# Kernel tuning notes

Measured on AMD Instinct MI355X. Metric: run time of the kernel, lower is better.

The kernel has to match this reference:

```python
import jax, jax.numpy as jnp
import numpy as np

N, H, W, C = 4, 64, 64, 256
G, K = 8, 3
GC = C // G
P = K * K
PAD = 1
BN_EPS = 1e-3  # ultralytics Conv uses BatchNorm2d(eps=0.001)


def setup_inputs() -> dict:
    key = jax.random.key(0)
    ks = jax.random.split(key, 8)
    return {
        "x": jax.random.normal(ks[0], (N, H, W, C), jnp.float32),
        # depthwise conv weight (OIHW with I=1, feature_group_count=C)
        "dw_w": jax.random.normal(ks[1], (C, 1, K, K), jnp.float32) * 0.1,
        "bn_gamma": jnp.ones((C,), jnp.float32),
        "bn_beta": jnp.zeros((C,), jnp.float32),
        "bn_mean": jnp.zeros((C,), jnp.float32),
        "bn_var": jnp.ones((C,), jnp.float32),
        # offset/mask heads are zero-init in torch; use small random weights so
        # sampling locations are nontrivial but stay near the kernel grid
        "W_off": jax.random.normal(ks[2], (C, G * P * 2), jnp.float32) * 0.01,
        "b_off": jnp.zeros((G * P * 2,), jnp.float32),
        "W_mask": jax.random.normal(ks[3], (C, G * P), jnp.float32) * 0.01,
        "b_mask": jnp.zeros((G * P,), jnp.float32),
        "W_in": jax.random.normal(ks[4], (C, C), jnp.float32) / np.sqrt(C).astype(np.float32),
        "b_in": jnp.zeros((C,), jnp.float32),
        "W_out": jax.random.normal(ks[5], (C, C), jnp.float32) / np.sqrt(C).astype(np.float32),
        "b_out": jnp.zeros((C,), jnp.float32),
    }


def _grid_sample(img, grid):
    # img: (B, gc, Hi, Wi); grid: (B, L, P, 2) in [-1,1], (x,y) order.
    # Matches torch grid_sample(mode='bilinear', padding_mode='zeros', align_corners=False).
    B, gc, Hi, Wi = img.shape
    x = (grid[..., 0] + 1.0) * (Wi * 0.5) - 0.5
    y = (grid[..., 1] + 1.0) * (Hi * 0.5) - 0.5
    x0 = jnp.floor(x).astype(jnp.int32)
    y0 = jnp.floor(y).astype(jnp.int32)
    tx = x - x0
    ty = y - y0
    flat = img.reshape(B, gc, Hi * Wi)
    L, Pp = grid.shape[1], grid.shape[2]

    def tap(xi, yi, w):
        valid = (xi >= 0) & (xi < Wi) & (yi >= 0) & (yi < Hi)
        idx = jnp.clip(yi, 0, Hi - 1) * Wi + jnp.clip(xi, 0, Wi - 1)
        v = jnp.take_along_axis(flat, idx.reshape(B, 1, L * Pp), axis=2)
        v = v.reshape(B, gc, L, Pp)
        return v * (w * valid)[:, None]

    return (tap(x0, y0, (1 - tx) * (1 - ty))
            + tap(x0 + 1, y0, tx * (1 - ty))
            + tap(x0, y0 + 1, (1 - tx) * ty)
            + tap(x0 + 1, y0 + 1, tx * ty))


def _dcnv3_core(xp, offset, mask):
    # xp: (N,H,W,C) projected input; offset: (N,H,W,G*P*2); mask: (N,H,W,G*P)
    xpad = jnp.pad(xp, ((0, 0), (PAD, PAD), (PAD, PAD), (0, 0)))
    Hi, Wi = H + 2 * PAD, W + 2 * PAD
    # reference points on the padded grid, normalized to [0,1]
    start = (K - 1) // 2 + 0.5  # dilation=1, stride=1
    ref_y = (start + jnp.arange(H, dtype=jnp.float32)) / Hi
    ref_x = (start + jnp.arange(W, dtype=jnp.float32)) / Wi
    ref = jnp.stack(jnp.broadcast_arrays(ref_x[None, :], ref_y[:, None]), -1)  # (H,W,2) (x,y)
    # kernel dilation grid; torch meshgrid('ij') over (kw,kh) -> point p = iw*K + ih
    xv = jnp.arange(K, dtype=jnp.float32) - ((K - 1) // 2)
    gx, gy = jnp.meshgrid(xv / Wi, xv / Hi, indexing='ij')
    kgrid = jnp.stack([gx, gy], -1).reshape(P, 2)  # identical per group
    off = offset.reshape(N, H, W, G, P, 2) / jnp.array([Wi, Hi], jnp.float32)
    loc = ref[None, :, :, None, None, :] + kgrid[None, None, None, None] + off  # (N,H,W,G,P,2)
    sg = 2.0 * loc - 1.0
    # regroup channels-last input to (N*G, GC, Hi, Wi); channel c = g*GC + d
    img = xpad.reshape(N, Hi * Wi, G, GC).transpose(0, 2, 3, 1).reshape(N * G, GC, Hi, Wi)
    sgrid = sg.reshape(N, H * W, G, P, 2).transpose(0, 2, 1, 3, 4).reshape(N * G, H * W, P, 2)
    samp = _grid_sample(img, sgrid)  # (N*G, GC, L, P)
    m = mask.reshape(N, H * W, G, P).transpose(0, 2, 1, 3).reshape(N * G, 1, H * W, P)
    out = (samp * m).sum(-1)  # (N*G, GC, L)
    return out.reshape(N, C, H * W).transpose(0, 2, 1).reshape(N, H, W, C)


def reference(x, dw_w, bn_gamma, bn_beta, bn_mean, bn_var, W_off, b_off,
              W_mask, b_mask, W_in, b_in, W_out, b_out):
    x_proj = x @ W_in + b_in
    # depthwise 3x3 conv + BN (eval) + SiLU (ultralytics Conv)
    xc = x.transpose(0, 3, 1, 2)
    y = jax.lax.conv_general_dilated(
        xc, dw_w, (1, 1), ((PAD, PAD), (PAD, PAD)),
        feature_group_count=C, dimension_numbers=('NCHW', 'OIHW', 'NCHW'))
    scale = bn_gamma / jnp.sqrt(bn_var + BN_EPS)
    y = (y - bn_mean[None, :, None, None]) * scale[None, :, None, None] + bn_beta[None, :, None, None]
    y = y * jax.nn.sigmoid(y)
    x1 = y.transpose(0, 2, 3, 1)  # (N,H,W,C)
    offset = x1 @ W_off + b_off
    mlog = (x1 @ W_mask + b_mask).reshape(N, H, W, G, P)
    mask = jax.nn.softmax(mlog, axis=-1).reshape(N, H, W, G * P)
    out = _dcnv3_core(x_proj, offset, mask)
    return out @ W_out + b_out
```

## Files before the change

kernel.cpp:

```cpp
#include <hip/hip_runtime.h>
#include <math.h>

#define NPIX 16384
#define CC 256
#define OFFW 144
#define MSKW 72

typedef unsigned short ushortT;
typedef __attribute__((ext_vector_type(4))) float f32x4;
typedef __attribute__((ext_vector_type(8))) short short8;
typedef __attribute__((ext_vector_type(8))) __bf16 bf16x8;

__device__ __forceinline__ float bf2f(ushortT u) {
    union { unsigned u; float f; } x; x.u = ((unsigned)u) << 16; return x.f;
}
__device__ __forceinline__ ushortT f2bf(float f) {
    union { float f; unsigned u; } x; x.f = f;
    unsigned u = x.u;
    return (ushortT)((u + 0x7FFFu + ((u >> 16) & 1u)) >> 16);
}

typedef __attribute__((address_space(3))) char lds_char;
typedef __attribute__((address_space(1))) char glb_char;
__device__ __forceinline__ void gload_lds16(const void* g, void* l) {
    __builtin_amdgcn_global_load_lds((const glb_char*)g, (lds_char*)l, 16, 0, 0);
}

__global__ __launch_bounds__(256) void k_wt(
    const float* __restrict__ W_in, const float* __restrict__ W_out,
    const float* __restrict__ W_off, const float* __restrict__ W_mask,
    const float* __restrict__ b_in, const float* __restrict__ b_out,
    const float* __restrict__ b_off, const float* __restrict__ b_mask,
    ushortT* __restrict__ Wt, float* __restrict__ biasb)
{
    const int idx = blockIdx.x * 256 + threadIdx.x;
    const int slot = idx >> 16;
    const int rem = idx & 65535;
    const int n = rem >> 8, k = rem & 255;
    float v;
    if (slot == 0)      v = W_in[k * 256 + n];
    else if (slot == 1) v = W_out[k * 256 + n];
    else {
        if (n < OFFW)            v = W_off[k * OFFW + n];
        else if (n < OFFW + MSKW) v = W_mask[k * MSKW + (n - OFFW)];
        else                     v = 0.f;
    }
    Wt[idx] = f2bf(v);
    if (n == 0) {
        float b;
        if (slot == 0)      b = b_in[k];
        else if (slot == 1) b = b_out[k];
        else                b = (k < OFFW) ? b_off[k] : (k < OFFW + MSKW ? b_mask[k - OFFW] : 0.f);
        biasb[slot * 256 + k] = b;
    }
}

__global__ __launch_bounds__(256) void k_pre(
    const float* __restrict__ x, const float* __restrict__ dw_w,
    const float* __restrict__ bn_gamma, const float* __restrict__ bn_beta,
    const float* __restrict__ bn_mean, const float* __restrict__ bn_var,
    ushortT* __restrict__ xb, ushortT* __restrict__ x1b)
{
    __shared__ float xs[30][CC];
    const int tid = threadIdx.x;
    const int base = blockIdx.x * 8;
    const int n = base >> 12, h = (base >> 6) & 63, w0 = base & 63;

    #pragma unroll
    for (int v = 0; v < 30; ++v) {
        const int r = h - 1 + v / 10;
        const int col = w0 - 1 + v % 10;
        float val = 0.f;
        if ((unsigned)r < 64u && (unsigned)col < 64u)
            val = x[(((size_t)n * 64 + r) * 64 + col) * CC + tid];
        xs[v][tid] = val;
    }
    __syncthreads();

    float wreg[9];
    #pragma unroll
    for (int kk = 0; kk < 9; ++kk) wreg[kk] = dw_w[tid * 9 + kk];
    const float scale = bn_gamma[tid] * rsqrtf(bn_var[tid] + 1e-3f);
    const float mean = bn_mean[tid], beta = bn_beta[tid];

    #pragma unroll
    for (int t = 0; t < 8; ++t) {
        float acc = 0.f;
        #pragma unroll
        for (int kh = 0; kh < 3; ++kh)
            #pragma unroll
            for (int kw = 0; kw < 3; ++kw)
                acc += xs[kh * 10 + t + kw][tid] * wreg[kh * 3 + kw];
        float yv = (acc - mean) * scale + beta;
        float s = yv / (1.f + __expf(-yv));
        x1b[(size_t)(base + t) * CC + tid] = f2bf(s);
        xb[(size_t)(base + t) * CC + tid] = f2bf(xs[10 + t + 1][tid]);
    }
}

template <int OUT_BF16>
__global__ __launch_bounds__(256) void k_gemm(
    const ushortT* __restrict__ A, const ushortT* __restrict__ Bt,
    const float* __restrict__ bias, void* __restrict__ Cout)
{
    __shared__ ushortT As[64 * 64];
    __shared__ ushortT Bs[64 * 64];
    const int tid = threadIdx.x;
    const int lane = tid & 63, wave = tid >> 6;
    const int mt = blockIdx.x >> 2, nt = blockIdx.x & 3;
    const int m0 = mt * 64, n0 = nt * 64;
    const int wr = wave >> 1, wc = wave & 1;

    f32x4 acc[2][2];
    #pragma unroll
    for (int i = 0; i < 2; ++i)
        #pragma unroll
        for (int j = 0; j < 2; ++j) acc[i][j] = (f32x4){0.f, 0.f, 0.f, 0.f};

    for (int k0 = 0; k0 < 256; k0 += 64) {
        #pragma unroll
        for (int it = 0; it < 2; ++it) {
            const int i = tid + it * 256;
            const int row = i >> 3, ch = i & 7;
            const int sch = ch ^ (row & 7);
            const int ldsoff = it * 4096 + wave * 1024;
            gload_lds16(A + (size_t)(m0 + row) * 256 + k0 + sch * 8, (char*)As + ldsoff);
            gload_lds16(Bt + (size_t)(n0 + row) * 256 + k0 + sch * 8, (char*)Bs + ldsoff);
        }
        __syncthreads();

        #pragma unroll
        for (int kk = 0; kk < 64; kk += 32) {
            bf16x8 af[2], bf[2];
            #pragma unroll
            for (int m = 0; m < 2; ++m) {
                const int rowl = wr * 32 + m * 16 + (lane & 15);
                const int colb = (kk + (lane >> 4) * 8) * 2;
                af[m] = *(const bf16x8*)((const char*)As + rowl * 128 + (colb ^ ((rowl & 7) << 4)));
            }
            #pragma unroll
            for (int nn = 0; nn < 2; ++nn) {
                const int rowl = wc * 32 + nn * 16 + (lane & 15);
                const int colb = (kk + (lane >> 4) * 8) * 2;
                bf[nn] = *(const bf16x8*)((const char*)Bs + rowl * 128 + (colb ^ ((rowl & 7) << 4)));
            }
            #pragma unroll
            for (int m = 0; m < 2; ++m)
                #pragma unroll
                for (int nn = 0; nn < 2; ++nn)
                    acc[m][nn] = __builtin_amdgcn_mfma_f32_16x16x32_bf16(af[m], bf[nn], acc[m][nn], 0, 0, 0);
        }
        __syncthreads();
    }

    const int rbase = (lane >> 4) * 4, col16 = lane & 15;
    #pragma unroll
    for (int m = 0; m < 2; ++m) {
        #pragma unroll
        for (int nn = 0; nn < 2; ++nn) {
            const int col = n0 + wc * 32 + nn * 16 + col16;
            const float bj = bias[col];
            #pragma unroll
            for (int r = 0; r < 4; ++r) {
                const int row = m0 + wr * 32 + m * 16 + rbase + r;
                const float v = acc[m][nn][r] + bj;
                if (OUT_BF16) ((ushortT*)Cout)[(size_t)row * 256 + col] = f2bf(v);
                else          ((float*)Cout)[(size_t)row * 256 + col] = v;
            }
        }
    }
}

__global__ __launch_bounds__(256) void k_core(
    const float* __restrict__ om, const ushortT* __restrict__ xpb,
    ushortT* __restrict__ coreb)
{
    __shared__ float offL[8][CC];
    __shared__ float msk[8][MSKW];
    __shared__ float wtab[576][8];
    const int tid = threadIdx.x;
    const int base = blockIdx.x * 8;
    const int n = base >> 12, h = (base >> 6) & 63, w0 = base & 63;

    for (int i = tid; i < 8 * CC; i += 256)
        offL[i >> 8][i & 255] = om[(size_t)base * CC + i];
    __syncthreads();

    if (tid < 64) {
        const int t = tid >> 3, g = tid & 7;
        float mx = -1e30f;
        #pragma unroll
        for (int p = 0; p < 9; ++p) mx = fmaxf(mx, offL[t][OFFW + g * 9 + p]);
        float e[9], sum = 0.f;
        #pragma unroll
        for (int p = 0; p < 9; ++p) { e[p] = __expf(offL[t][OFFW + g * 9 + p] - mx); sum += e[p]; }
        const float inv = 1.f / sum;
        #pragma unroll
        for (int p = 0; p < 9; ++p) msk[t][g * 9 + p] = e[p] * inv;
    }
    __syncthreads();

    for (int it = tid; it < 576; it += 256) {
        const int t = it / 72, gp = it % 72, p = gp % 9;
        const float ox = offL[t][gp * 2], oy = offL[t][gp * 2 + 1];
        const float m = msk[t][gp];
        const float px = (float)(w0 + t + p / 3) + ox;
        const float py = (float)(h + p % 3) + oy;
        const float xf = floorf(px), yf = floorf(py);
        const float tx = px - xf, ty = py - yf;
        const int x0 = (int)xf - 1, y0 = (int)yf - 1;
        const int x1 = x0 + 1, y1 = y0 + 1;
        const float wx0 = ((unsigned)x0 < 64u) ? (1.f - tx) : 0.f;
        const float wx1 = ((unsigned)x1 < 64u) ? tx : 0.f;
        const float wy0 = ((unsigned)y0 < 64u) ? (1.f - ty) : 0.f;
        const float wy1 = ((unsigned)y1 < 64u) ? ty : 0.f;
        const int cx0 = min(max(x0, 0), 63), cx1 = min(max(x1, 0), 63);
        const int cy0 = min(max(y0, 0), 63), cy1 = min(max(y1, 0), 63);
        wtab[it][0] = __int_as_float((cy0 * 64 + cx0) * 256);
        wtab[it][1] = __int_as_float((cy0 * 64 + cx1) * 256);
        wtab[it][2] = __int_as_float((cy1 * 64 + cx0) * 256);
        wtab[it][3] = __int_as_float((cy1 * 64 + cx1) * 256);
        wtab[it][4] = m * wx0 * wy0;
        wtab[it][5] = m * wx1 * wy0;
        wtab[it][6] = m * wx0 * wy1;
        wtab[it][7] = m * wx1 * wy1;
    }
    __syncthreads();

    const int g = tid >> 5, d = tid & 31;
    const int c = g * 32 + d;
    const ushortT* xn = xpb + (size_t)n * 4096 * 256 + c;
    #pragma unroll
    for (int t = 0; t < 8; ++t) {
        float acc = 0.f;
        #pragma unroll
        for (int p = 0; p < 9; ++p) {
            const float* wt = wtab[t * 72 + g * 9 + p];
            const int4 o4 = *(const int4*)(wt);
            const float4 w4 = *(const float4*)(wt + 4);
            acc += w4.x * bf2f(xn[o4.x]) + w4.y * bf2f(xn[o4.y])
                 + w4.z * bf2f(xn[o4.z]) + w4.w * bf2f(xn[o4.w]);
        }
        coreb[(size_t)(base + t) * CC + c] = f2bf(acc);
    }
}

extern "C" void kernel_launch(void* const* d_in, const int* in_sizes, int n_in,
                              void* d_out, int out_size, void* d_ws, size_t ws_size,
                              hipStream_t stream) {
    const float* x        = (const float*)d_in[0];
    const float* dw_w     = (const float*)d_in[1];
    const float* bn_gamma = (const float*)d_in[2];
    const float* bn_beta  = (const float*)d_in[3];
    const float* bn_mean  = (const float*)d_in[4];
    const float* bn_var   = (const float*)d_in[5];
    const float* W_off    = (const float*)d_in[6];
    const float* b_off    = (const float*)d_in[7];
    const float* W_mask   = (const float*)d_in[8];
    const float* b_mask   = (const float*)d_in[9];
    const float* W_in     = (const float*)d_in[10];
    const float* b_in     = (const float*)d_in[11];
    const float* W_out    = (const float*)d_in[12];
    const float* b_out    = (const float*)d_in[13];
    float* out = (float*)d_out;

    char* w = (char*)d_ws;
    ushortT* Wt   = (ushortT*)w;
    float* biasb  = (float*)(w + 393216);
    ushortT* xb   = (ushortT*)(w + 396288);
    ushortT* x1b  = (ushortT*)(w + 396288 + 8388608);
    ushortT* xpb  = (ushortT*)(w + 396288 + 2 * 8388608);
    float* om     = (float*)(w + 396288 + 3 * 8388608);
    ushortT* coreb = x1b;

    hipLaunchKernelGGL(k_wt, dim3(768), dim3(256), 0, stream,
                       W_in, W_out, W_off, W_mask, b_in, b_out, b_off, b_mask, Wt, biasb);
    hipLaunchKernelGGL(k_pre, dim3(NPIX / 8), dim3(256), 0, stream,
                       x, dw_w, bn_gamma, bn_beta, bn_mean, bn_var, xb, x1b);
    hipLaunchKernelGGL((k_gemm<0>), dim3(NPIX / 64 * 4), dim3(256), 0, stream,
                       x1b, Wt + 2 * 65536, biasb + 2 * 256, (void*)om);
    hipLaunchKernelGGL((k_gemm<1>), dim3(NPIX / 64 * 4), dim3(256), 0, stream,
                       xb, Wt, biasb, (void*)xpb);
    hipLaunchKernelGGL(k_core, dim3(NPIX / 8), dim3(256), 0, stream,
                       om, xpb, coreb);
    hipLaunchKernelGGL((k_gemm<0>), dim3(NPIX / 64 * 4), dim3(256), 0, stream,
                       coreb, Wt + 65536, biasb + 256, (void*)out);
}
```

Baseline: 77.53 us.

## Fuse depthwise conv with input GEMMs and sampling core with output GEMM

Replaces the six-kernel pipeline with three kernels. One kernel per image row computes the depthwise conv, BN and SiLU into LDS, then runs both the input projection and the offset/mask GEMMs from LDS. A second kernel runs softmax, deformable sampling and the output GEMM per 16 pixels. This removes the intermediate bf16 tensors for x, x1 and core from global memory, along with extra launches. In exchange, B operands are read straight from global memory with no LDS staging, and the first kernel runs only 256 large blocks, which may leave the GPU underoccupied.

```diff
diff --git a/kernel.cpp b/kernel.cpp
--- a/kernel.cpp
+++ b/kernel.cpp
@@ -8,8 +8,8 @@
 
 typedef unsigned short ushortT;
 typedef __attribute__((ext_vector_type(4))) float f32x4;
-typedef __attribute__((ext_vector_type(8))) short short8;
 typedef __attribute__((ext_vector_type(8))) __bf16 bf16x8;
+typedef __attribute__((ext_vector_type(4))) unsigned short u16x4;
 
 __device__ __forceinline__ float bf2f(ushortT u) {
     union { unsigned u; float f; } x; x.u = ((unsigned)u) << 16; return x.f;
@@ -18,12 +18,6 @@
     union { float f; unsigned u; } x; x.f = f;
     unsigned u = x.u;
     return (ushortT)((u + 0x7FFFu + ((u >> 16) & 1u)) >> 16);
-}
-
-typedef __attribute__((address_space(3))) char lds_char;
-typedef __attribute__((address_space(1))) char glb_char;
-__device__ __forceinline__ void gload_lds16(const void* g, void* l) {
-    __builtin_amdgcn_global_load_lds((const glb_char*)g, (lds_char*)l, 16, 0, 0);
 }
 
 __global__ __launch_bounds__(256) void k_wt(
@@ -41,9 +35,9 @@
     if (slot == 0)      v = W_in[k * 256 + n];
     else if (slot == 1) v = W_out[k * 256 + n];
     else {
-        if (n < OFFW)            v = W_off[k * OFFW + n];
+        if (n < OFFW)             v = W_off[k * OFFW + n];
         else if (n < OFFW + MSKW) v = W_mask[k * MSKW + (n - OFFW)];
-        else                     v = 0.f;
+        else                      v = 0.f;
     }
     Wt[idx] = f2bf(v);
     if (n == 0) {
@@ -55,193 +49,243 @@
     }
 }
 
-__global__ __launch_bounds__(256) void k_pre(
+__device__ __forceinline__ void gemm_acc64(const ushortT* __restrict__ As,
+                                           const ushortT* __restrict__ Bt,
+                                           int lane, int wr, int wc, f32x4 acc[2][4])
+{
+    #pragma unroll
+    for (int k0 = 0; k0 < 256; k0 += 32) {
+        bf16x8 af[2], bb[4];
+        #pragma unroll
+        for (int m = 0; m < 2; ++m) {
+            const int row = wr * 32 + m * 16 + (lane & 15);
+            af[m] = *(const bf16x8*)((const char*)As + row * 512 +
+                     (((k0 + (lane >> 4) * 8) * 2) ^ ((row & 7) << 4)));
+        }
+        #pragma unroll
+        for (int nn = 0; nn < 4; ++nn) {
+            const int ncol = wc * 64 + nn * 16 + (lane & 15);
+            bb[nn] = *(const bf16x8*)(Bt + (size_t)ncol * 256 + k0 + (lane >> 4) * 8);
+        }
+        #pragma unroll
+        for (int m = 0; m < 2; ++m)
+            #pragma unroll
+            for (int nn = 0; nn < 4; ++nn)
+                acc[m][nn] = __builtin_amdgcn_mfma_f32_16x16x32_bf16(af[m], bb[nn], acc[m][nn], 0, 0, 0);
+    }
+}
+
+__global__ __launch_bounds__(512, 2) void k_fused_in(
     const float* __restrict__ x, const float* __restrict__ dw_w,
     const float* __restrict__ bn_gamma, const float* __restrict__ bn_beta,
     const float* __restrict__ bn_mean, const float* __restrict__ bn_var,
-    ushortT* __restrict__ xb, ushortT* __restrict__ x1b)
+    const ushortT* __restrict__ Wt, const float* __restrict__ biasb,
+    ushortT* __restrict__ xpb, float* __restrict__ om)
 {
-    __shared__ float xs[30][CC];
+    __shared__ __align__(16) ushortT xA[64 * 256];
+    __shared__ __align__(16) ushortT x1s[64 * 256];
     const int tid = threadIdx.x;
-    const int base = blockIdx.x * 8;
+    const int b0 = blockIdx.x;
+    const int lb = (b0 & 7) * 32 + (b0 >> 3);
+    const int n = lb >> 6, h = lb & 63;
+    const int basepix = lb * 64;
+    const float* xrow = x + (size_t)basepix * 256;
+
+    #pragma unroll
+    for (int i = 0; i < 8; ++i) {
+        const int eid = i * 512 + tid;
+        const int w = eid >> 6, c4 = (eid & 63) << 2;
+        const float4 v = *(const float4*)(xrow + w * 256 + c4);
+        u16x4 u; u[0] = f2bf(v.x); u[1] = f2bf(v.y); u[2] = f2bf(v.z); u[3] = f2bf(v.w);
+        *(u16x4*)((char*)xA + ((w * 512 + c4 * 2) ^ ((w & 7) << 4))) = u;
+    }
+
+    {
+        const int c = tid & 255, half = tid >> 8;
+        float wreg[9];
+        #pragma unroll
+        for (int k = 0; k < 9; ++k) wreg[k] = dw_w[c * 9 + k];
+        const float scale = bn_gamma[c] * rsqrtf(bn_var[c] + 1e-3f);
+        const float mean = bn_mean[c], beta = bn_beta[c];
+        const bool hv0 = (h - 1) >= 0, hv2 = (h + 1) < 64;
+        const float* r0 = x + (((size_t)(n * 64 + h - 1)) * 64) * 256 + c;
+        const float* r1 = x + (((size_t)(n * 64 + h)) * 64) * 256 + c;
+        const float* r2 = x + (((size_t)(n * 64 + h + 1)) * 64) * 256 + c;
+        const int w0 = half * 32;
+        float a0, a1, a2, e0, e1, e2, d0, d1, d2;
+        if (w0 - 1 >= 0) {
+            a0 = hv0 ? r0[(w0 - 1) * 256] : 0.f;
+            a1 = r1[(w0 - 1) * 256];
+            a2 = hv2 ? r2[(w0 - 1) * 256] : 0.f;
+        } else { a0 = a1 = a2 = 0.f; }
+        e0 = hv0 ? r0[w0 * 256] : 0.f;
+        e1 = r1[w0 * 256];
+        e2 = hv2 ? r2[w0 * 256] : 0.f;
+        for (int w = w0; w < w0 + 32; ++w) {
+            if (w + 1 < 64) {
+                d0 = hv0 ? r0[(w + 1) * 256] : 0.f;
+                d1 = r1[(w + 1) * 256];
+                d2 = hv2 ? r2[(w + 1) * 256] : 0.f;
+            } else { d0 = d1 = d2 = 0.f; }
+            float acc = a0 * wreg[0] + e0 * wreg[1] + d0 * wreg[2]
+                      + a1 * wreg[3] + e1 * wreg[4] + d1 * wreg[5]
+                      + a2 * wreg[6] + e2 * wreg[7] + d2 * wreg[8];
+            const float yv = (acc - mean) * scale + beta;
+            const float s = yv / (1.f + __expf(-yv));
+            *(ushortT*)((char*)x1s + ((w * 512 + c * 2) ^ ((w & 7) << 4))) = f2bf(s);
+            a0 = e0; a1 = e1; a2 = e2;
+            e0 = d0; e1 = d1; e2 = d2;
+        }
+    }
+    __syncthreads();
+
+    const int lane = tid & 63, wave = tid >> 6;
+    const int wr = wave >> 2, wc = wave & 3;
+    const int rbase = (lane >> 4) * 4, col16 = lane & 15;
+
+    {
+        f32x4 acc[2][4];
+        #pragma unroll
+        for (int m = 0; m < 2; ++m)
+            #pragma unroll
+            for (int nn = 0; nn < 4; ++nn) acc[m][nn] = (f32x4){0.f, 0.f, 0.f, 0.f};
+        gemm_acc64(xA, Wt, lane, wr, wc, acc);
+        #pragma unroll
+        for (int m = 0; m < 2; ++m)
+            #pragma unroll
+            for (int nn = 0; nn < 4; ++nn) {
+                const int col = wc * 64 + nn * 16 + col16;
+                const float bj = biasb[col];
+                #pragma unroll
+                for (int r = 0; r < 4; ++r) {
+                    const int row = wr * 32 + m * 16 + rbase + r;
+                    xpb[(size_t)(basepix + row) * 256 + col] = f2bf(acc[m][nn][r] + bj);
+                }
+            }
+    }
+    {
+        f32x4 acc[2][4];
+        #pragma unroll
+        for (int m = 0; m < 2; ++m)
+            #pragma unroll
+            for (int nn = 0; nn < 4; ++nn) acc[m][nn] = (f32x4){0.f, 0.f, 0.f, 0.f};
+        gemm_acc64(x1s, Wt + 2 * 65536, lane, wr, wc, acc);
+        #pragma unroll
+        for (int m = 0; m < 2; ++m)
+            #pragma unroll
+            for (int nn = 0; nn < 4; ++nn) {
+                const int col = wc * 64 + nn * 16 + col16;
+                const float bj = biasb[512 + col];
+                #pragma unroll
+                for (int r = 0; r < 4; ++r) {
+                    const int row = wr * 32 + m * 16 + rbase + r;
+                    om[(size_t)(basepix + row) * 256 + col] = acc[m][nn][r] + bj;
+                }
+            }
+    }
+}
+
+__global__ __launch_bounds__(256, 4) void k_fused_out(
+    const float* __restrict__ om, const ushortT* __restrict__ xpb,
+    const ushortT* __restrict__ Wt1, const float* __restrict__ bias1,
+    float* __restrict__ out)
+{
+    __shared__ __align__(16) float wtab[16][72][8];
+    __shared__ __align__(16) ushortT core[16 * 256];
+    const int tid = threadIdx.x;
+    const int b0 = blockIdx.x;
+    const int lb = (b0 & 7) * 128 + (b0 >> 3);
+    const int base = lb * 16;
     const int n = base >> 12, h = (base >> 6) & 63, w0 = base & 63;
 
-    #pragma unroll
-    for (int v = 0; v < 30; ++v) {
-        const int r = h - 1 + v / 10;
-        const int col = w0 - 1 + v % 10;
-        float val = 0.f;
-        if ((unsigned)r < 64u && (unsigned)col < 64u)
-            val = x[(((size_t)n * 64 + r) * 64 + col) * CC + tid];
-        xs[v][tid] = val;
+    if (tid < 128) {
+        const int px = tid >> 3, g = tid & 7;
+        const float* omp = om + (size_t)(base + px) * 256;
+        float lg[9], mx = -1e30f;
+        #pragma unroll
+        for (int p = 0; p < 9; ++p) { lg[p] = omp[OFFW + g * 9 + p]; mx = fmaxf(mx, lg[p]); }
+        float e[9], sum = 0.f;
+        #pragma unroll
+        for (int p = 0; p < 9; ++p) { e[p] = __expf(lg[p] - mx); sum += e[p]; }
+        const float inv = 1.f / sum;
+        #pragma unroll
+        for (int p = 0; p < 9; ++p) {
+            const float m = e[p] * inv;
+            const float ox = omp[(g * 9 + p) * 2], oy = omp[(g * 9 + p) * 2 + 1];
+            const float pxc = (float)(w0 + px + p / 3) + ox;
+            const float pyc = (float)(h + p % 3) + oy;
+            const float xf = floorf(pxc), yf = floorf(pyc);
+            const float tx = pxc - xf, ty = pyc - yf;
+            const int x0 = (int)xf - 1, y0 = (int)yf - 1;
+            const int x1 = x0 + 1, y1 = y0 + 1;
+            const float wx0 = ((unsigned)x0 < 64u) ? (1.f - tx) : 0.f;
+            const float wx1 = ((unsigned)x1 < 64u) ? tx : 0.f;
+            const float wy0 = ((unsigned)y0 < 64u) ? (1.f - ty) : 0.f;
+            const float wy1 = ((unsigned)y1 < 64u) ? ty : 0.f;
+            const int cx0 = min(max(x0, 0), 63), cx1 = min(max(x1, 0), 63);
+            const int cy0 = min(max(y0, 0), 63), cy1 = min(max(y1, 0), 63);
+            float* dst = wtab[px][g * 9 + p];
+            float4 idx4, wt4;
+            idx4.x = __int_as_float((cy0 * 64 + cx0) * 256);
+            idx4.y = __int_as_float((cy0 * 64 + cx1) * 256);
+            idx4.z = __int_as_float((cy1 * 64 + cx0) * 256);
+            idx4.w = __int_as_float((cy1 * 64 + cx1) * 256);
+            wt4.x = m * wx0 * wy0; wt4.y = m * wx1 * wy0;
+            wt4.z = m * wx0 * wy1; wt4.w = m * wx1 * wy1;
+            *(float4*)dst = idx4;
+            *(float4*)(dst + 4) = wt4;
+        }
     }
     __syncthreads();
 
-    float wreg[9];
-    #pragma unroll
-    for (int kk = 0; kk < 9; ++kk) wreg[kk] = dw_w[tid * 9 + kk];
-    const float scale = bn_gamma[tid] * rsqrtf(bn_var[tid] + 1e-3f);
-    const float mean = bn_mean[tid], beta = bn_beta[tid];
-
-    #pragma unroll
-    for (int t = 0; t < 8; ++t) {
-        float acc = 0.f;
-        #pragma unroll
-        for (int kh = 0; kh < 3; ++kh)
-            #pragma unroll
-            for (int kw = 0; kw < 3; ++kw)
-                acc += xs[kh * 10 + t + kw][tid] * wreg[kh * 3 + kw];
-        float yv = (acc - mean) * scale + beta;
-        float s = yv / (1.f + __expf(-yv));
-        x1b[(size_t)(base + t) * CC + tid] = f2bf(s);
-        xb[(size_t)(base + t) * CC + tid] = f2bf(xs[10 + t + 1][tid]);
-    }
-}
-
-template <int OUT_BF16>
-__global__ __launch_bounds__(256) void k_gemm(
-    const ushortT* __restrict__ A, const ushortT* __restrict__ Bt,
-    const float* __restrict__ bias, void* __restrict__ Cout)
-{
-    __shared__ ushortT As[64 * 64];
-    __shared__ ushortT Bs[64 * 64];
-    const int tid = threadIdx.x;
+    {
+        const int g = tid >> 5, d = tid & 31;
+        const int c = g * 32 + d;
+        const ushortT* xn = xpb + (size_t)n * (4096 * 256) + c;
+        #pragma unroll 2
+        for (int px = 0; px < 16; ++px) {
+            float acc = 0.f;
+            #pragma unroll
+            for (int p = 0; p < 9; ++p) {
+                const float* wt = wtab[px][g * 9 + p];
+                const int4 o4 = *(const int4*)(wt);
+                const float4 w4 = *(const float4*)(wt + 4);
+                acc += w4.x * bf2f(xn[o4.x]) + w4.y * bf2f(xn[o4.y])
+                     + w4.z * bf2f(xn[o4.z]) + w4.w * bf2f(xn[o4.w]);
+            }
+            *(ushortT*)((char*)core + ((px * 512 + c * 2) ^ ((px & 7) << 4))) = f2bf(acc);
+        }
+    }
+    __syncthreads();
+
     const int lane = tid & 63, wave = tid >> 6;
-    const int mt = blockIdx.x >> 2, nt = blockIdx.x & 3;
-    const int m0 = mt * 64, n0 = nt * 64;
-    const int wr = wave >> 1, wc = wave & 1;
-
-    f32x4 acc[2][2];
-    #pragma unroll
-    for (int i = 0; i < 2; ++i)
-        #pragma unroll
-        for (int j = 0; j < 2; ++j) acc[i][j] = (f32x4){0.f, 0.f, 0.f, 0.f};
-
-    for (int k0 = 0; k0 < 256; k0 += 64) {
-        #pragma unroll
-        for (int it = 0; it < 2; ++it) {
-            const int i = tid + it * 256;
-            const int row = i >> 3, ch = i & 7;
-            const int sch = ch ^ (row & 7);
-            const int ldsoff = it * 4096 + wave * 1024;
-            gload_lds16(A + (size_t)(m0 + row) * 256 + k0 + sch * 8, (char*)As + ldsoff);
-            gload_lds16(Bt + (size_t)(n0 + row) * 256 + k0 + sch * 8, (char*)Bs + ldsoff);
-        }
-        __syncthreads();
-
-        #pragma unroll
-        for (int kk = 0; kk < 64; kk += 32) {
-            bf16x8 af[2], bf[2];
-            #pragma unroll
-            for (int m = 0; m < 2; ++m) {
-                const int rowl = wr * 32 + m * 16 + (lane & 15);
-                const int colb = (kk + (lane >> 4) * 8) * 2;
-                af[m] = *(const bf16x8*)((const char*)As + rowl * 128 + (colb ^ ((rowl & 7) << 4)));
-            }
-            #pragma unroll
-            for (int nn = 0; nn < 2; ++nn) {
-                const int rowl = wc * 32 + nn * 16 + (lane & 15);
-                const int colb = (kk + (lane >> 4) * 8) * 2;
-                bf[nn] = *(const bf16x8*)((const char*)Bs + rowl * 128 + (colb ^ ((rowl & 7) << 4)));
-            }
-            #pragma unroll
-            for (int m = 0; m < 2; ++m)
-                #pragma unroll
-                for (int nn = 0; nn < 2; ++nn)
-                    acc[m][nn] = __builtin_amdgcn_mfma_f32_16x16x32_bf16(af[m], bf[nn], acc[m][nn], 0, 0, 0);
-        }
-        __syncthreads();
-    }
-
+    f32x4 acc[4];
+    #pragma unroll
+    for (int nn = 0; nn < 4; ++nn) acc[nn] = (f32x4){0.f, 0.f, 0.f, 0.f};
+    #pragma unroll
+    for (int k0 = 0; k0 < 256; k0 += 32) {
+        const int row = lane & 15;
+        const bf16x8 af = *(const bf16x8*)((const char*)core + row * 512 +
+                           (((k0 + (lane >> 4) * 8) * 2) ^ ((row & 7) << 4)));
+        bf16x8 bb[4];
+        #pragma unroll
+        for (int nn = 0; nn < 4; ++nn) {
+            const int ncol = wave * 64 + nn * 16 + (lane & 15);
+            bb[nn] = *(const bf16x8*)(Wt1 + (size_t)ncol * 256 + k0 + (lane >> 4) * 8);
+        }
+        #pragma unroll
+        for (int nn = 0; nn < 4; ++nn)
+            acc[nn] = __builtin_amdgcn_mfma_f32_16x16x32_bf16(af, bb[nn], acc[nn], 0, 0, 0);
+    }
     const int rbase = (lane >> 4) * 4, col16 = lane & 15;
     #pragma unroll
-    for (int m = 0; m < 2; ++m) {
-        #pragma unroll
-        for (int nn = 0; nn < 2; ++nn) {
-            const int col = n0 + wc * 32 + nn * 16 + col16;
-            const float bj = bias[col];
-            #pragma unroll
-            for (int r = 0; r < 4; ++r) {
-                const int row = m0 + wr * 32 + m * 16 + rbase + r;
-                const float v = acc[m][nn][r] + bj;
-                if (OUT_BF16) ((ushortT*)Cout)[(size_t)row * 256 + col] = f2bf(v);
-                else          ((float*)Cout)[(size_t)row * 256 + col] = v;
-            }
-        }
-    }
-}
-
-__global__ __launch_bounds__(256) void k_core(
-    const float* __restrict__ om, const ushortT* __restrict__ xpb,
-    ushortT* __restrict__ coreb)
-{
-    __shared__ float offL[8][CC];
-    __shared__ float msk[8][MSKW];
-    __shared__ float wtab[576][8];
-    const int tid = threadIdx.x;
-    const int base = blockIdx.x * 8;
-    const int n = base >> 12, h = (base >> 6) & 63, w0 = base & 63;
-
-    for (int i = tid; i < 8 * CC; i += 256)
-        offL[i >> 8][i & 255] = om[(size_t)base * CC + i];
-    __syncthreads();
-
-    if (tid < 64) {
-        const int t = tid >> 3, g = tid & 7;
-        float mx = -1e30f;
-        #pragma unroll
-        for (int p = 0; p < 9; ++p) mx = fmaxf(mx, offL[t][OFFW + g * 9 + p]);
-        float e[9], sum = 0.f;
-        #pragma unroll
-        for (int p = 0; p < 9; ++p) { e[p] = __expf(offL[t][OFFW + g * 9 + p] - mx); sum += e[p]; }
-        const float inv = 1.f / sum;
-        #pragma unroll
-        for (int p = 0; p < 9; ++p) msk[t][g * 9 + p] = e[p] * inv;
-    }
-    __syncthreads();
-
-    for (int it = tid; it < 576; it += 256) {
-        const int t = it / 72, gp = it % 72, p = gp % 9;
-        const float ox = offL[t][gp * 2], oy = offL[t][gp * 2 + 1];
-        const float m = msk[t][gp];
-        const float px = (float)(w0 + t + p / 3) + ox;
-        const float py = (float)(h + p % 3) + oy;
-        const float xf = floorf(px), yf = floorf(py);
-        const float tx = px - xf, ty = py - yf;
-        const int x0 = (int)xf - 1, y0 = (int)yf - 1;
-        const int x1 = x0 + 1, y1 = y0 + 1;
-        const float wx0 = ((unsigned)x0 < 64u) ? (1.f - tx) : 0.f;
-        const float wx1 = ((unsigned)x1 < 64u) ? tx : 0.f;
-        const float wy0 = ((unsigned)y0 < 64u) ? (1.f - ty) : 0.f;
-        const float wy1 = ((unsigned)y1 < 64u) ? ty : 0.f;
-        const int cx0 = min(max(x0, 0), 63), cx1 = min(max(x1, 0), 63);
-        const int cy0 = min(max(y0, 0), 63), cy1 = min(max(y1, 0), 63);
-        wtab[it][0] = __int_as_float((cy0 * 64 + cx0) * 256);
-        wtab[it][1] = __int_as_float((cy0 * 64 + cx1) * 256);
-        wtab[it][2] = __int_as_float((cy1 * 64 + cx0) * 256);
-        wtab[it][3] = __int_as_float((cy1 * 64 + cx1) * 256);
-        wtab[it][4] = m * wx0 * wy0;
-        wtab[it][5] = m * wx1 * wy0;
-        wtab[it][6] = m * wx0 * wy1;
-        wtab[it][7] = m * wx1 * wy1;
-    }
-    __syncthreads();
-
-    const int g = tid >> 5, d = tid & 31;
-    const int c = g * 32 + d;
-    const ushortT* xn = xpb + (size_t)n * 4096 * 256 + c;
-    #pragma unroll
-    for (int t = 0; t < 8; ++t) {
-        float acc = 0.f;
-        #pragma unroll
-        for (int p = 0; p < 9; ++p) {
-            const float* wt = wtab[t * 72 + g * 9 + p];
-            const int4 o4 = *(const int4*)(wt);
-            const float4 w4 = *(const float4*)(wt + 4);
-            acc += w4.x * bf2f(xn[o4.x]) + w4.y * bf2f(xn[o4.y])
-                 + w4.z * bf2f(xn[o4.z]) + w4.w * bf2f(xn[o4.w]);
-        }
-        coreb[(size_t)(base + t) * CC + c] = f2bf(acc);
+    for (int nn = 0; nn < 4; ++nn) {
+        const int col = wave * 64 + nn * 16 + col16;
+        const float bj = bias1[col];
+        #pragma unroll
+        for (int r = 0; r < 4; ++r) {
+            out[(size_t)(base + rbase + r) * 256 + col] = acc[nn][r] + bj;
+        }
     }
 }
 
@@ -267,22 +311,13 @@
     char* w = (char*)d_ws;
     ushortT* Wt   = (ushortT*)w;
     float* biasb  = (float*)(w + 393216);
-    ushortT* xb   = (ushortT*)(w + 396288);
-    ushortT* x1b  = (ushortT*)(w + 396288 + 8388608);
-    ushortT* xpb  = (ushortT*)(w + 396288 + 2 * 8388608);
-    float* om     = (float*)(w + 396288 + 3 * 8388608);
-    ushortT* coreb = x1b;
+    ushortT* xpb  = (ushortT*)(w + 396288);
+    float* om     = (float*)(w + 396288 + 8388608);
 
     hipLaunchKernelGGL(k_wt, dim3(768), dim3(256), 0, stream,
                        W_in, W_out, W_off, W_mask, b_in, b_out, b_off, b_mask, Wt, biasb);
-    hipLaunchKernelGGL(k_pre, dim3(NPIX / 8), dim3(256), 0, stream,
-                       x, dw_w, bn_gamma, bn_beta, bn_mean, bn_var, xb, x1b);
-    hipLaunchKernelGGL((k_gemm<0>), dim3(NPIX / 64 * 4), dim3(256), 0, stream,
-                       x1b, Wt + 2 * 65536, biasb + 2 * 256, (void*)om);
-    hipLaunchKernelGGL((k_gemm<1>), dim3(NPIX / 64 * 4), dim3(256), 0, stream,
-                       xb, Wt, biasb, (void*)xpb);
-    hipLaunchKernelGGL(k_core, dim3(NPIX / 8), dim3(256), 0, stream,
-                       om, xpb, coreb);
-    hipLaunchKernelGGL((k_gemm<0>), dim3(NPIX / 64 * 4), dim3(256), 0, stream,
-                       coreb, Wt + 65536, biasb + 256, (void*)out);
-}
+    hipLaunchKernelGGL(k_fused_in, dim3(256), dim3(512), 0, stream,
+                       x, dw_w, bn_gamma, bn_beta, bn_mean, bn_var, Wt, biasb, xpb, om);
+    hipLaunchKernelGGL(k_fused_out, dim3(1024), dim3(256), 0, stream,
+                       om, xpb, Wt + 65536, biasb + 256, out);
+}
```

Measured after the change: 146.6 us. 89.1% more time.
